# Kernel tuning notes

Hardware: AMD Instinct MI355X
Metric: run time of the kernel (lower is better)

The kernel has to match this reference:

```python
import jax, jax.numpy as jnp
import numpy as np

B, S, D = 4, 512, 256
VOCAB, MAX_RULES = 50257, 1024
EPS = 1e-12  # F.normalize default eps


def setup_inputs() -> dict:
    key = jax.random.key(0)
    k1, k2, k3, k4 = jax.random.split(key, 4)
    hidden_states = jax.random.normal(k1, (B, S, D), dtype=jnp.float32)
    token_ids = jax.random.randint(k2, (B, S), 0, VOCAB, dtype=jnp.int64)
    rule_transform = jax.random.normal(k3, (MAX_RULES, D, D), dtype=jnp.float32)
    token_rules = jax.random.randint(k4, (VOCAB,), 0, MAX_RULES, dtype=jnp.int64)
    return {
        "hidden_states": hidden_states,
        "token_ids": token_ids,
        "rule_transform": rule_transform,
        "token_rules": token_rules,
    }


def reference(hidden_states, token_ids, rule_transform, token_rules):
    # per-token rule index: [B, S]
    rule_indices = token_rules[token_ids]
    # gather DxD rule matrix per token: [B, S, D, D]
    rule_matrices = rule_transform[rule_indices]
    # F.normalize(p=2, dim=(-2,-1)): divide by Frobenius norm per matrix
    fro = jnp.sqrt(jnp.sum(rule_matrices * rule_matrices, axis=(-2, -1), keepdims=True))
    rule_matrices = rule_matrices / jnp.maximum(fro, EPS)
    # batched matvec: [B,S,D] x [B,S,D,E] -> [B,S,E]
    return jnp.einsum("bsd,bsde->bse", hidden_states, rule_matrices)
```

## Files before the change

### kernel.cpp

```cpp
#include <hip/hip_runtime.h>
#include <math.h>

#define D 256
#define NRULES 1024
#define TPB 8
#define KMAX 16

__global__ void prep_kernel(const int* __restrict__ token_ids,
                            const int* __restrict__ token_rules,
                            int ntok,
                            int* __restrict__ counts,
                            int* __restrict__ bucket,
                            int* __restrict__ spill,
                            int* __restrict__ nspill) {
    const int i = blockIdx.x * blockDim.x + threadIdx.x;
    if (i >= ntok) return;
    const int r = token_rules[token_ids[i]];
    const int slot = atomicAdd(&counts[r], 1);
    if (slot < KMAX) bucket[r * KMAX + slot] = i;
    else             spill[atomicAdd(nspill, 1)] = (r << 16) | i;
}

__device__ __forceinline__ void apply_rule(
    const float* __restrict__ M,
    const int* toks,
    int count,
    const float* __restrict__ hidden,
    float* __restrict__ out,
    float (*h_lds)[D], float* sq_lds,
    int t, int wave, int lane, int rr, int col)
{
    for (int base = 0; base < count; base += TPB) {
        #pragma unroll
        for (int j = 0; j < TPB; ++j) {
            const int idx = base + j;
            h_lds[j][t] = (idx < count)
                ? hidden[(size_t)toks[idx] * D + t] : 0.f;
        }
        __syncthreads();

        float4 acc[TPB];
        #pragma unroll
        for (int j = 0; j < TPB; ++j) acc[j] = float4{0.f, 0.f, 0.f, 0.f};
        float sq = 0.f;

        #pragma unroll 8
        for (int i = 0; i < 64; ++i) {
            const int d = (i << 2) + rr;
            const float4 m = *reinterpret_cast<const float4*>(M + (size_t)d * D + col);
            sq = fmaf(m.x, m.x, fmaf(m.y, m.y, fmaf(m.z, m.z, fmaf(m.w, m.w, sq))));
            #pragma unroll
            for (int j = 0; j < TPB; ++j) {
                const float h = h_lds[j][d];
                acc[j].x = fmaf(h, m.x, acc[j].x);
                acc[j].y = fmaf(h, m.y, acc[j].y);
                acc[j].z = fmaf(h, m.z, acc[j].z);
                acc[j].w = fmaf(h, m.w, acc[j].w);
            }
        }

        #pragma unroll
        for (int off = 32; off > 0; off >>= 1)
            sq += __shfl_down(sq, off, 64);
        if (lane == 0) sq_lds[wave] = sq;

        #pragma unroll
        for (int j = 0; j < TPB; ++j) {
            #pragma unroll
            for (int mask = 16; mask < 64; mask <<= 1) {
                acc[j].x += __shfl_xor(acc[j].x, mask, 64);
                acc[j].y += __shfl_xor(acc[j].y, mask, 64);
                acc[j].z += __shfl_xor(acc[j].z, mask, 64);
                acc[j].w += __shfl_xor(acc[j].w, mask, 64);
            }
        }
        __syncthreads();

        const float fro2 = sq_lds[0] + sq_lds[1] + sq_lds[2] + sq_lds[3];
        const float inv  = 1.0f / fmaxf(sqrtf(fro2), 1e-12f);

        #pragma unroll
        for (int j = 0; j < TPB; ++j) {
            if (rr == (j & 3) && base + j < count) {
                const int tok = toks[base + j];
                float4 o;
                o.x = acc[j].x * inv; o.y = acc[j].y * inv;
                o.z = acc[j].z * inv; o.w = acc[j].w * inv;
                *reinterpret_cast<float4*>(out + (size_t)tok * D + col) = o;
            }
        }
        __syncthreads();
    }
}

__global__ __launch_bounds__(256) void process_kernel(
    const float* __restrict__ hidden,
    const float* __restrict__ rules,
    const int*   __restrict__ counts,
    const int*   __restrict__ bucket,
    const int*   __restrict__ spill,
    const int*   __restrict__ nspill,
    float* __restrict__ out)
{
    const int b    = blockIdx.x;
    const int t    = threadIdx.x;
    const int wave = t >> 6;
    const int lane = t & 63;
    const int rr   = lane >> 4;
    const int col  = (wave << 6) + ((lane & 15) << 2);

    __shared__ float h_lds[TPB][D];
    __shared__ float sq_lds[4];
    __shared__ int   toks[KMAX];

    const int cnt = min(counts[b], KMAX);
    if (cnt > 0) {
        if (t < cnt) toks[t] = bucket[b * KMAX + t];
        __syncthreads();
        apply_rule(rules + (size_t)b * D * D, toks, cnt,
                   hidden, out, h_lds, sq_lds, t, wave, lane, rr, col);
    }

    const int ns = nspill[0];
    for (int k = b; k < ns; k += gridDim.x) {
        __syncthreads();
        const int e = spill[k];
        if (t == 0) toks[0] = e & 0xFFFF;
        __syncthreads();
        apply_rule(rules + (size_t)(e >> 16) * D * D, toks, 1,
                   hidden, out, h_lds, sq_lds, t, wave, lane, rr, col);
    }
}

extern "C" void kernel_launch(void* const* d_in, const int* in_sizes, int n_in,
                              void* d_out, int out_size, void* d_ws, size_t ws_size,
                              hipStream_t stream) {
    const float* hidden      = (const float*)d_in[0];
    const int*   token_ids   = (const int*)d_in[1];
    const float* rules       = (const float*)d_in[2];
    const int*   token_rules = (const int*)d_in[3];
    float*       out         = (float*)d_out;

    const int ntok = in_sizes[1];

    int* ws     = (int*)d_ws;
    int* counts = ws;
    int* nspill = ws + NRULES;
    int* bucket = ws + NRULES + 8;
    int* spill  = bucket + NRULES * KMAX;

    hipMemsetAsync(counts, 0, (NRULES + 8) * sizeof(int), stream);
    prep_kernel<<<(ntok + 255) / 256, 256, 0, stream>>>(
        token_ids, token_rules, ntok, counts, bucket, spill, nspill);
    process_kernel<<<NRULES, 256, 0, stream>>>(
        hidden, rules, counts, bucket, spill, nspill, out);
}
```

Before: 50.74 us.

## Split per-rule work into column-quarter units with compacted worklist and separate norm pass

The prep kernel now builds a compacted worklist of (rule, column-quarter) units, so only rules that have tokens launch blocks, and each 64-thread block handles a quarter of the output columns. The Frobenius norm is accumulated per quarter into a buffer and applied by a new elementwise normalization kernel. Compute loops are templated on the actual token count to avoid wasted FMAs on padded slots. The aim is to drop idle blocks, raise parallelism and cut useless work. The cost is an extra kernel launch and an extra read/write pass over the output. The grid size is fixed at 4*NRULES+256, which can cap the number of spill units.

```diff
diff --git a/kernel.cpp b/kernel.cpp
--- a/kernel.cpp
+++ b/kernel.cpp
@@ -11,31 +11,100 @@
                             int ntok,
                             int* __restrict__ counts,
                             int* __restrict__ bucket,
-                            int* __restrict__ spill,
-                            int* __restrict__ nspill) {
+                            int* __restrict__ rule_of_token,
+                            int* __restrict__ worklist,
+                            int* __restrict__ nunits) {
     const int i = blockIdx.x * blockDim.x + threadIdx.x;
     if (i >= ntok) return;
     const int r = token_rules[token_ids[i]];
+    rule_of_token[i] = r;
     const int slot = atomicAdd(&counts[r], 1);
-    if (slot < KMAX) bucket[r * KMAX + slot] = i;
-    else             spill[atomicAdd(nspill, 1)] = (r << 16) | i;
-}
-
-__device__ __forceinline__ void apply_rule(
-    const float* __restrict__ M,
-    const int* toks,
-    int count,
+    if (slot < KMAX) {
+        bucket[r * KMAX + slot] = i;
+        if (slot == 0) {
+            const int w = atomicAdd(nunits, 4);
+            #pragma unroll
+            for (int q = 0; q < 4; ++q) worklist[w + q] = (r << 2) | q;
+        }
+    } else {
+        const int w = atomicAdd(nunits, 4);
+        #pragma unroll
+        for (int q = 0; q < 4; ++q)
+            worklist[w + q] = (int)(0x80000000u | ((unsigned)i << 2) | (unsigned)q);
+    }
+}
+
+template <int CNT>
+__device__ __forceinline__ void quarter_compute(
+    const float* __restrict__ M, const float (*__restrict__ h_lds)[D],
+    int rr, int col, float4* acc, float& sq)
+{
+    #pragma unroll 8
+    for (int i = 0; i < 64; ++i) {
+        const int d = (i << 2) + rr;
+        const float4 m = *reinterpret_cast<const float4*>(M + (size_t)d * D + col);
+        sq = fmaf(m.x, m.x, fmaf(m.y, m.y, fmaf(m.z, m.z, fmaf(m.w, m.w, sq))));
+        #pragma unroll
+        for (int j = 0; j < CNT; ++j) {
+            const float h = h_lds[j][d];
+            acc[j].x = fmaf(h, m.x, acc[j].x);
+            acc[j].y = fmaf(h, m.y, acc[j].y);
+            acc[j].z = fmaf(h, m.z, acc[j].z);
+            acc[j].w = fmaf(h, m.w, acc[j].w);
+        }
+    }
+}
+
+__global__ __launch_bounds__(64) void matvec_kernel(
     const float* __restrict__ hidden,
-    float* __restrict__ out,
-    float (*h_lds)[D], float* sq_lds,
-    int t, int wave, int lane, int rr, int col)
+    const float* __restrict__ rules,
+    const int*   __restrict__ counts,
+    const int*   __restrict__ bucket,
+    const int*   __restrict__ rule_of_token,
+    const int*   __restrict__ worklist,
+    const int*   __restrict__ nunits,
+    float* __restrict__ fro2buf,
+    float* __restrict__ out)
 {
-    for (int base = 0; base < count; base += TPB) {
-        #pragma unroll
-        for (int j = 0; j < TPB; ++j) {
-            const int idx = base + j;
-            h_lds[j][t] = (idx < count)
-                ? hidden[(size_t)toks[idx] * D + t] : 0.f;
+    if ((int)blockIdx.x >= nunits[0]) return;
+    const int e  = worklist[blockIdx.x];
+    const int t  = threadIdx.x;
+    const int rr = t >> 4;
+    const int c4 = (t & 15) << 2;
+
+    __shared__ float h_lds[TPB][D];
+    __shared__ int   toks[KMAX];
+
+    int r, q, cnt;
+    bool owner;
+    if (e < 0) {
+        const int tok = (e & 0x7fffffff) >> 2;
+        q = e & 3;
+        r = rule_of_token[tok];
+        cnt = 1;
+        owner = false;
+        if (t == 0) toks[0] = tok;
+    } else {
+        r = e >> 2; q = e & 3;
+        cnt = min(counts[r], KMAX);
+        owner = true;
+        if (t < cnt) toks[t] = bucket[r * KMAX + t];
+    }
+    __syncthreads();
+
+    const int col = (q << 6) + c4;
+    const float* __restrict__ M = rules + (size_t)r * D * D;
+
+    for (int base = 0; base < cnt; base += TPB) {
+        const int c  = min(cnt - base, TPB);
+        const int cr = (c == 1) ? 1 : (c == 2) ? 2 : (c <= 4) ? 4 : 8;
+
+        for (int j = 0; j < cr; ++j) {
+            float4 v = {0.f, 0.f, 0.f, 0.f};
+            if (j < c)
+                v = *reinterpret_cast<const float4*>(
+                    &hidden[(size_t)toks[base + j] * D + (t << 2)]);
+            *reinterpret_cast<float4*>(&h_lds[j][t << 2]) = v;
         }
         __syncthreads();
 
@@ -44,28 +113,14 @@
         for (int j = 0; j < TPB; ++j) acc[j] = float4{0.f, 0.f, 0.f, 0.f};
         float sq = 0.f;
 
-        #pragma unroll 8
-        for (int i = 0; i < 64; ++i) {
-            const int d = (i << 2) + rr;
-            const float4 m = *reinterpret_cast<const float4*>(M + (size_t)d * D + col);
-            sq = fmaf(m.x, m.x, fmaf(m.y, m.y, fmaf(m.z, m.z, fmaf(m.w, m.w, sq))));
-            #pragma unroll
-            for (int j = 0; j < TPB; ++j) {
-                const float h = h_lds[j][d];
-                acc[j].x = fmaf(h, m.x, acc[j].x);
-                acc[j].y = fmaf(h, m.y, acc[j].y);
-                acc[j].z = fmaf(h, m.z, acc[j].z);
-                acc[j].w = fmaf(h, m.w, acc[j].w);
-            }
-        }
-
-        #pragma unroll
-        for (int off = 32; off > 0; off >>= 1)
-            sq += __shfl_down(sq, off, 64);
-        if (lane == 0) sq_lds[wave] = sq;
-
-        #pragma unroll
-        for (int j = 0; j < TPB; ++j) {
+        switch (cr) {
+            case 1: quarter_compute<1>(M, h_lds, rr, col, acc, sq); break;
+            case 2: quarter_compute<2>(M, h_lds, rr, col, acc, sq); break;
+            case 4: quarter_compute<4>(M, h_lds, rr, col, acc, sq); break;
+            default: quarter_compute<8>(M, h_lds, rr, col, acc, sq); break;
+        }
+
+        for (int j = 0; j < cr; ++j) {
             #pragma unroll
             for (int mask = 16; mask < 64; mask <<= 1) {
                 acc[j].x += __shfl_xor(acc[j].x, mask, 64);
@@ -74,62 +129,42 @@
                 acc[j].w += __shfl_xor(acc[j].w, mask, 64);
             }
         }
+
+        if (owner && base == 0) {
+            float s = sq;
+            #pragma unroll
+            for (int off = 32; off > 0; off >>= 1)
+                s += __shfl_down(s, off, 64);
+            if (t == 0) fro2buf[(r << 2) | q] = s;
+        }
+
+        for (int j = 0; j < cr; ++j) {
+            if (j < c && rr == (j & 3)) {
+                const int tok = toks[base + j];
+                *reinterpret_cast<float4*>(&out[(size_t)tok * D + col]) = acc[j];
+            }
+        }
         __syncthreads();
-
-        const float fro2 = sq_lds[0] + sq_lds[1] + sq_lds[2] + sq_lds[3];
-        const float inv  = 1.0f / fmaxf(sqrtf(fro2), 1e-12f);
-
-        #pragma unroll
-        for (int j = 0; j < TPB; ++j) {
-            if (rr == (j & 3) && base + j < count) {
-                const int tok = toks[base + j];
-                float4 o;
-                o.x = acc[j].x * inv; o.y = acc[j].y * inv;
-                o.z = acc[j].z * inv; o.w = acc[j].w * inv;
-                *reinterpret_cast<float4*>(out + (size_t)tok * D + col) = o;
-            }
-        }
-        __syncthreads();
-    }
-}
-
-__global__ __launch_bounds__(256) void process_kernel(
-    const float* __restrict__ hidden,
-    const float* __restrict__ rules,
-    const int*   __restrict__ counts,
-    const int*   __restrict__ bucket,
-    const int*   __restrict__ spill,
-    const int*   __restrict__ nspill,
-    float* __restrict__ out)
+    }
+}
+
+__global__ __launch_bounds__(256) void norm_kernel(
+    float* __restrict__ out,
+    const int* __restrict__ rule_of_token,
+    const float* __restrict__ fro2buf,
+    int ntok)
 {
-    const int b    = blockIdx.x;
-    const int t    = threadIdx.x;
-    const int wave = t >> 6;
-    const int lane = t & 63;
-    const int rr   = lane >> 4;
-    const int col  = (wave << 6) + ((lane & 15) << 2);
-
-    __shared__ float h_lds[TPB][D];
-    __shared__ float sq_lds[4];
-    __shared__ int   toks[KMAX];
-
-    const int cnt = min(counts[b], KMAX);
-    if (cnt > 0) {
-        if (t < cnt) toks[t] = bucket[b * KMAX + t];
-        __syncthreads();
-        apply_rule(rules + (size_t)b * D * D, toks, cnt,
-                   hidden, out, h_lds, sq_lds, t, wave, lane, rr, col);
-    }
-
-    const int ns = nspill[0];
-    for (int k = b; k < ns; k += gridDim.x) {
-        __syncthreads();
-        const int e = spill[k];
-        if (t == 0) toks[0] = e & 0xFFFF;
-        __syncthreads();
-        apply_rule(rules + (size_t)(e >> 16) * D * D, toks, 1,
-                   hidden, out, h_lds, sq_lds, t, wave, lane, rr, col);
-    }
+    const int g   = blockIdx.x * 256 + threadIdx.x;
+    const int tok = g >> 6;
+    if (tok >= ntok) return;
+    const int c4  = (g & 63) << 2;
+    const int r   = rule_of_token[tok];
+    const float f = fro2buf[r * 4] + fro2buf[r * 4 + 1] +
+                    fro2buf[r * 4 + 2] + fro2buf[r * 4 + 3];
+    const float inv = 1.0f / fmaxf(sqrtf(f), 1e-12f);
+    float4 v = *reinterpret_cast<float4*>(&out[(size_t)tok * D + c4]);
+    v.x *= inv; v.y *= inv; v.z *= inv; v.w *= inv;
+    *reinterpret_cast<float4*>(&out[(size_t)tok * D + c4]) = v;
 }
 
 extern "C" void kernel_launch(void* const* d_in, const int* in_sizes, int n_in,
@@ -143,15 +178,23 @@
 
     const int ntok = in_sizes[1];
 
-    int* ws     = (int*)d_ws;
-    int* counts = ws;
-    int* nspill = ws + NRULES;
-    int* bucket = ws + NRULES + 8;
-    int* spill  = bucket + NRULES * KMAX;
+    int* ws            = (int*)d_ws;
+    int* counts        = ws;
+    int* nunits        = ws + NRULES;
+    int* bucket        = ws + NRULES + 8;
+    int* rule_of_token = bucket + NRULES * KMAX;
+    int* worklist      = rule_of_token + ntok;
+    float* fro2buf     = (float*)(worklist + 4 * NRULES + 1024);
+
+    const int max_units = 4 * NRULES + 256;
 
     hipMemsetAsync(counts, 0, (NRULES + 8) * sizeof(int), stream);
     prep_kernel<<<(ntok + 255) / 256, 256, 0, stream>>>(
-        token_ids, token_rules, ntok, counts, bucket, spill, nspill);
-    process_kernel<<<NRULES, 256, 0, stream>>>(
-        hidden, rules, counts, bucket, spill, nspill, out);
-}
+        token_ids, token_rules, ntok, counts, bucket, rule_of_token,
+        worklist, nunits);
+    matvec_kernel<<<max_units, 64, 0, stream>>>(
+        hidden, rules, counts, bucket, rule_of_token, worklist, nunits,
+        fro2buf, out);
+    norm_kernel<<<(ntok * 64 + 255) / 256, 256, 0, stream>>>(
+        out, rule_of_token, fro2buf, ntok);
+}
```

New measurement: 82.37 us. 1.62x slower.

## Use single-wave blocks with count-specialized rule passes and extra spill blocks

Applied to the files above, without the earlier changes.

Shrinks each per-rule block from four waves to one 64-thread wave that walks all 256 rows, so the cross-wave shuffle reductions and LDS exchange of the squared norm go away. Templates the inner pass on the token count (1/2/4/8) so rules with few tokens avoid wasted FMAs on zero-padded rows. Adds extra blocks dedicated to spilled tokens. In exchange each block streams the whole 256 KB matrix with one wave, which lowers per-block memory-level parallelism and may leave the GPU underfilled.

```diff
diff --git a/kernel.cpp b/kernel.cpp
--- a/kernel.cpp
+++ b/kernel.cpp
@@ -5,6 +5,7 @@
 #define NRULES 1024
 #define TPB 8
 #define KMAX 16
+#define NSPILLBLK 64
 
 __global__ void prep_kernel(const int* __restrict__ token_ids,
                             const int* __restrict__ token_rules,
@@ -21,79 +22,56 @@
     else             spill[atomicAdd(nspill, 1)] = (r << 16) | i;
 }
 
-__device__ __forceinline__ void apply_rule(
+template <int CNT>
+__device__ __forceinline__ void rule_pass(
     const float* __restrict__ M,
-    const int* toks,
-    int count,
-    const float* __restrict__ hidden,
-    float* __restrict__ out,
-    float (*h_lds)[D], float* sq_lds,
-    int t, int wave, int lane, int rr, int col)
+    const float (*__restrict__ h_lds)[D],
+    const int* __restrict__ toks,
+    int c,
+    int t,
+    float* __restrict__ out)
 {
-    for (int base = 0; base < count; base += TPB) {
+    const int c4 = t << 2;
+    float4 acc[CNT];
+    #pragma unroll
+    for (int j = 0; j < CNT; ++j) acc[j] = float4{0.f, 0.f, 0.f, 0.f};
+    float sqx = 0.f, sqy = 0.f, sqz = 0.f, sqw = 0.f;
+
+    #pragma unroll 8
+    for (int d = 0; d < D; ++d) {
+        const float4 m = *reinterpret_cast<const float4*>(M + (size_t)d * D + c4);
+        sqx = fmaf(m.x, m.x, sqx);
+        sqy = fmaf(m.y, m.y, sqy);
+        sqz = fmaf(m.z, m.z, sqz);
+        sqw = fmaf(m.w, m.w, sqw);
         #pragma unroll
-        for (int j = 0; j < TPB; ++j) {
-            const int idx = base + j;
-            h_lds[j][t] = (idx < count)
-                ? hidden[(size_t)toks[idx] * D + t] : 0.f;
+        for (int j = 0; j < CNT; ++j) {
+            const float h = h_lds[j][d];
+            acc[j].x = fmaf(h, m.x, acc[j].x);
+            acc[j].y = fmaf(h, m.y, acc[j].y);
+            acc[j].z = fmaf(h, m.z, acc[j].z);
+            acc[j].w = fmaf(h, m.w, acc[j].w);
         }
-        __syncthreads();
+    }
 
-        float4 acc[TPB];
-        #pragma unroll
-        for (int j = 0; j < TPB; ++j) acc[j] = float4{0.f, 0.f, 0.f, 0.f};
-        float sq = 0.f;
+    float sq = (sqx + sqy) + (sqz + sqw);
+    #pragma unroll
+    for (int mask = 1; mask < 64; mask <<= 1)
+        sq += __shfl_xor(sq, mask, 64);
+    const float inv = 1.0f / fmaxf(sqrtf(sq), 1e-12f);
 
-        #pragma unroll 8
-        for (int i = 0; i < 64; ++i) {
-            const int d = (i << 2) + rr;
-            const float4 m = *reinterpret_cast<const float4*>(M + (size_t)d * D + col);
-            sq = fmaf(m.x, m.x, fmaf(m.y, m.y, fmaf(m.z, m.z, fmaf(m.w, m.w, sq))));
-            #pragma unroll
-            for (int j = 0; j < TPB; ++j) {
-                const float h = h_lds[j][d];
-                acc[j].x = fmaf(h, m.x, acc[j].x);
-                acc[j].y = fmaf(h, m.y, acc[j].y);
-                acc[j].z = fmaf(h, m.z, acc[j].z);
-                acc[j].w = fmaf(h, m.w, acc[j].w);
-            }
+    #pragma unroll
+    for (int j = 0; j < CNT; ++j) {
+        if (j < c) {
+            float4 o;
+            o.x = acc[j].x * inv; o.y = acc[j].y * inv;
+            o.z = acc[j].z * inv; o.w = acc[j].w * inv;
+            *reinterpret_cast<float4*>(&out[(size_t)toks[j] * D + c4]) = o;
         }
-
-        #pragma unroll
-        for (int off = 32; off > 0; off >>= 1)
-            sq += __shfl_down(sq, off, 64);
-        if (lane == 0) sq_lds[wave] = sq;
-
-        #pragma unroll
-        for (int j = 0; j < TPB; ++j) {
-            #pragma unroll
-            for (int mask = 16; mask < 64; mask <<= 1) {
-                acc[j].x += __shfl_xor(acc[j].x, mask, 64);
-                acc[j].y += __shfl_xor(acc[j].y, mask, 64);
-                acc[j].z += __shfl_xor(acc[j].z, mask, 64);
-                acc[j].w += __shfl_xor(acc[j].w, mask, 64);
-            }
-        }
-        __syncthreads();
-
-        const float fro2 = sq_lds[0] + sq_lds[1] + sq_lds[2] + sq_lds[3];
-        const float inv  = 1.0f / fmaxf(sqrtf(fro2), 1e-12f);
-
-        #pragma unroll
-        for (int j = 0; j < TPB; ++j) {
-            if (rr == (j & 3) && base + j < count) {
-                const int tok = toks[base + j];
-                float4 o;
-                o.x = acc[j].x * inv; o.y = acc[j].y * inv;
-                o.z = acc[j].z * inv; o.w = acc[j].w * inv;
-                *reinterpret_cast<float4*>(out + (size_t)tok * D + col) = o;
-            }
-        }
-        __syncthreads();
     }
 }
 
-__global__ __launch_bounds__(256) void process_kernel(
+__global__ __launch_bounds__(64) void process_kernel(
     const float* __restrict__ hidden,
     const float* __restrict__ rules,
     const int*   __restrict__ counts,
@@ -102,33 +80,51 @@
     const int*   __restrict__ nspill,
     float* __restrict__ out)
 {
-    const int b    = blockIdx.x;
-    const int t    = threadIdx.x;
-    const int wave = t >> 6;
-    const int lane = t & 63;
-    const int rr   = lane >> 4;
-    const int col  = (wave << 6) + ((lane & 15) << 2);
+    const int b = blockIdx.x;
+    const int t = threadIdx.x;
 
     __shared__ float h_lds[TPB][D];
-    __shared__ float sq_lds[4];
-    __shared__ int   toks[KMAX];
+    __shared__ int   toks[TPB];
 
-    const int cnt = min(counts[b], KMAX);
-    if (cnt > 0) {
-        if (t < cnt) toks[t] = bucket[b * KMAX + t];
-        __syncthreads();
-        apply_rule(rules + (size_t)b * D * D, toks, cnt,
-                   hidden, out, h_lds, sq_lds, t, wave, lane, rr, col);
+    if (b < NRULES) {
+        const int cnt = min(counts[b], KMAX);
+        if (cnt > 0) {
+            const float* __restrict__ M = rules + (size_t)b * D * D;
+            for (int base = 0; base < cnt; base += TPB) {
+                const int c = min(cnt - base, TPB);
+                if (t < c) toks[t] = bucket[b * KMAX + base + t];
+                #pragma unroll
+                for (int j = 0; j < TPB; ++j) {
+                    float4 v = {0.f, 0.f, 0.f, 0.f};
+                    if (j < c)
+                        v = *reinterpret_cast<const float4*>(
+                            &hidden[(size_t)bucket[b * KMAX + base + j] * D + (t << 2)]);
+                    *reinterpret_cast<float4*>(&h_lds[j][t << 2]) = v;
+                }
+                __syncthreads();
+
+                switch ((c == 1) ? 1 : (c == 2) ? 2 : (c <= 4) ? 4 : 8) {
+                    case 1:  rule_pass<1>(M, h_lds, toks, c, t, out); break;
+                    case 2:  rule_pass<2>(M, h_lds, toks, c, t, out); break;
+                    case 4:  rule_pass<4>(M, h_lds, toks, c, t, out); break;
+                    default: rule_pass<8>(M, h_lds, toks, c, t, out); break;
+                }
+                __syncthreads();
+            }
+        }
     }
 
     const int ns = nspill[0];
     for (int k = b; k < ns; k += gridDim.x) {
         __syncthreads();
-        const int e = spill[k];
-        if (t == 0) toks[0] = e & 0xFFFF;
+        const int e   = spill[k];
+        const int tok = e & 0xFFFF;
+        const int r   = e >> 16;
+        if (t == 0) toks[0] = tok;
+        *reinterpret_cast<float4*>(&h_lds[0][t << 2]) =
+            *reinterpret_cast<const float4*>(&hidden[(size_t)tok * D + (t << 2)]);
         __syncthreads();
-        apply_rule(rules + (size_t)(e >> 16) * D * D, toks, 1,
-                   hidden, out, h_lds, sq_lds, t, wave, lane, rr, col);
+        rule_pass<1>(rules + (size_t)r * D * D, h_lds, toks, 1, t, out);
     }
 }
 
@@ -152,6 +148,6 @@
     hipMemsetAsync(counts, 0, (NRULES + 8) * sizeof(int), stream);
     prep_kernel<<<(ntok + 255) / 256, 256, 0, stream>>>(
         token_ids, token_rules, ntok, counts, bucket, spill, nspill);
-    process_kernel<<<NRULES, 256, 0, stream>>>(
+    process_kernel<<<NRULES + NSPILLBLK, 64, 0, stream>>>(
         hidden, rules, counts, bucket, spill, nspill, out);
 }
```

After: 111.0 us. +118.8%, slower.

## Add atomic worklist of active rules and count-specialized tile passes

Applied to the files above, without the earlier changes.

The prep kernel now records each rule that has tokens into a compact worklist. The process kernel has blocks pull rules from it through an atomic counter instead of launching one block per rule, so empty rules cost nothing. Per-pass token tiles are templated on actual count (1/2/4/8), which cuts wasted FMAs and registers when a rule has few tokens, and hidden loads become float4 wide. The cost is a global atomic per work item, a larger code footprint from template instantiations, and a work-stealing loop that only pays off when many rules are empty or lightly loaded.

```diff
diff --git a/kernel.cpp b/kernel.cpp
--- a/kernel.cpp
+++ b/kernel.cpp
@@ -11,86 +11,91 @@
                             int ntok,
                             int* __restrict__ counts,
                             int* __restrict__ bucket,
-                            int* __restrict__ spill,
-                            int* __restrict__ nspill) {
+                            int* __restrict__ worklist,
+                            int* __restrict__ ctrl,
+                            int* __restrict__ spill) {
     const int i = blockIdx.x * blockDim.x + threadIdx.x;
     if (i >= ntok) return;
     const int r = token_rules[token_ids[i]];
     const int slot = atomicAdd(&counts[r], 1);
-    if (slot < KMAX) bucket[r * KMAX + slot] = i;
-    else             spill[atomicAdd(nspill, 1)] = (r << 16) | i;
+    if (slot < KMAX) {
+        bucket[r * KMAX + slot] = i;
+        if (slot == 0) worklist[atomicAdd(&ctrl[0], 1)] = r;
+    } else {
+        spill[atomicAdd(&ctrl[2], 1)] = (r << 16) | i;
+    }
 }
 
-__device__ __forceinline__ void apply_rule(
+template <int CR>
+__device__ __forceinline__ void do_pass(
     const float* __restrict__ M,
-    const int* toks,
-    int count,
     const float* __restrict__ hidden,
-    float* __restrict__ out,
-    float (*h_lds)[D], float* sq_lds,
-    int t, int wave, int lane, int rr, int col)
+    const int* bucketrow,
+    int base, int c,
+    int t, int wave, int lane, int rr, int col,
+    float (*__restrict__ h_lds)[D], float* __restrict__ sq_lds,
+    float* __restrict__ out)
 {
-    for (int base = 0; base < count; base += TPB) {
+    for (int j = wave; j < CR; j += 4) {
+        float4 v = {0.f, 0.f, 0.f, 0.f};
+        if (j < c)
+            v = *reinterpret_cast<const float4*>(
+                &hidden[(size_t)bucketrow[base + j] * D + (lane << 2)]);
+        *reinterpret_cast<float4*>(&h_lds[j][lane << 2]) = v;
+    }
+    __syncthreads();
+
+    float4 acc[CR];
+    #pragma unroll
+    for (int j = 0; j < CR; ++j) acc[j] = float4{0.f, 0.f, 0.f, 0.f};
+    float sq = 0.f;
+
+    #pragma unroll 8
+    for (int i = 0; i < 64; ++i) {
+        const int d = (i << 2) + rr;
+        const float4 m = *reinterpret_cast<const float4*>(M + (size_t)d * D + col);
+        sq = fmaf(m.x, m.x, fmaf(m.y, m.y, fmaf(m.z, m.z, fmaf(m.w, m.w, sq))));
         #pragma unroll
-        for (int j = 0; j < TPB; ++j) {
-            const int idx = base + j;
-            h_lds[j][t] = (idx < count)
-                ? hidden[(size_t)toks[idx] * D + t] : 0.f;
+        for (int j = 0; j < CR; ++j) {
+            const float h = h_lds[j][d];
+            acc[j].x = fmaf(h, m.x, acc[j].x);
+            acc[j].y = fmaf(h, m.y, acc[j].y);
+            acc[j].z = fmaf(h, m.z, acc[j].z);
+            acc[j].w = fmaf(h, m.w, acc[j].w);
         }
-        __syncthreads();
+    }
 
-        float4 acc[TPB];
+    #pragma unroll
+    for (int off = 32; off > 0; off >>= 1)
+        sq += __shfl_down(sq, off, 64);
+    if (lane == 0) sq_lds[wave] = sq;
+
+    #pragma unroll
+    for (int j = 0; j < CR; ++j) {
         #pragma unroll
-        for (int j = 0; j < TPB; ++j) acc[j] = float4{0.f, 0.f, 0.f, 0.f};
-        float sq = 0.f;
+        for (int mask = 16; mask < 64; mask <<= 1) {
+            acc[j].x += __shfl_xor(acc[j].x, mask, 64);
+            acc[j].y += __shfl_xor(acc[j].y, mask, 64);
+            acc[j].z += __shfl_xor(acc[j].z, mask, 64);
+            acc[j].w += __shfl_xor(acc[j].w, mask, 64);
+        }
+    }
+    __syncthreads();
 
-        #pragma unroll 8
-        for (int i = 0; i < 64; ++i) {
-            const int d = (i << 2) + rr;
-            const float4 m = *reinterpret_cast<const float4*>(M + (size_t)d * D + col);
-            sq = fmaf(m.x, m.x, fmaf(m.y, m.y, fmaf(m.z, m.z, fmaf(m.w, m.w, sq))));
-            #pragma unroll
-            for (int j = 0; j < TPB; ++j) {
-                const float h = h_lds[j][d];
-                acc[j].x = fmaf(h, m.x, acc[j].x);
-                acc[j].y = fmaf(h, m.y, acc[j].y);
-                acc[j].z = fmaf(h, m.z, acc[j].z);
-                acc[j].w = fmaf(h, m.w, acc[j].w);
-            }
+    const float fro2 = sq_lds[0] + sq_lds[1] + sq_lds[2] + sq_lds[3];
+    const float inv  = 1.0f / fmaxf(sqrtf(fro2), 1e-12f);
+
+    #pragma unroll
+    for (int j = 0; j < CR; ++j) {
+        if (j < c && rr == (j & 3)) {
+            const int tok = bucketrow[base + j];
+            float4 o;
+            o.x = acc[j].x * inv; o.y = acc[j].y * inv;
+            o.z = acc[j].z * inv; o.w = acc[j].w * inv;
+            *reinterpret_cast<float4*>(&out[(size_t)tok * D + col]) = o;
         }
-
-        #pragma unroll
-        for (int off = 32; off > 0; off >>= 1)
-            sq += __shfl_down(sq, off, 64);
-        if (lane == 0) sq_lds[wave] = sq;
-
-        #pragma unroll
-        for (int j = 0; j < TPB; ++j) {
-            #pragma unroll
-            for (int mask = 16; mask < 64; mask <<= 1) {
-                acc[j].x += __shfl_xor(acc[j].x, mask, 64);
-                acc[j].y += __shfl_xor(acc[j].y, mask, 64);
-                acc[j].z += __shfl_xor(acc[j].z, mask, 64);
-                acc[j].w += __shfl_xor(acc[j].w, mask, 64);
-            }
-        }
-        __syncthreads();
-
-        const float fro2 = sq_lds[0] + sq_lds[1] + sq_lds[2] + sq_lds[3];
-        const float inv  = 1.0f / fmaxf(sqrtf(fro2), 1e-12f);
-
-        #pragma unroll
-        for (int j = 0; j < TPB; ++j) {
-            if (rr == (j & 3) && base + j < count) {
-                const int tok = toks[base + j];
-                float4 o;
-                o.x = acc[j].x * inv; o.y = acc[j].y * inv;
-                o.z = acc[j].z * inv; o.w = acc[j].w * inv;
-                *reinterpret_cast<float4*>(out + (size_t)tok * D + col) = o;
-            }
-        }
-        __syncthreads();
     }
+    __syncthreads();
 }
 
 __global__ __launch_bounds__(256) void process_kernel(
@@ -98,11 +103,11 @@
     const float* __restrict__ rules,
     const int*   __restrict__ counts,
     const int*   __restrict__ bucket,
+    const int*   __restrict__ worklist,
+    int*         __restrict__ ctrl,
     const int*   __restrict__ spill,
-    const int*   __restrict__ nspill,
     float* __restrict__ out)
 {
-    const int b    = blockIdx.x;
     const int t    = threadIdx.x;
     const int wave = t >> 6;
     const int lane = t & 63;
@@ -111,24 +116,40 @@
 
     __shared__ float h_lds[TPB][D];
     __shared__ float sq_lds[4];
-    __shared__ int   toks[KMAX];
+    __shared__ int   sh_w;
+    __shared__ int   stok[1];
 
-    const int cnt = min(counts[b], KMAX);
-    if (cnt > 0) {
-        if (t < cnt) toks[t] = bucket[b * KMAX + t];
+    const int nwork = ctrl[0];
+
+    for (;;) {
+        if (t == 0) sh_w = atomicAdd(&ctrl[1], 1);
         __syncthreads();
-        apply_rule(rules + (size_t)b * D * D, toks, cnt,
-                   hidden, out, h_lds, sq_lds, t, wave, lane, rr, col);
+        const int w = sh_w;
+        if (w >= nwork) break;
+
+        const int r   = worklist[w];
+        const int cnt = min(counts[r], KMAX);
+        const float* __restrict__ M = rules + (size_t)r * D * D;
+        const int* brow = &bucket[r * KMAX];
+
+        for (int base = 0; base < cnt; base += TPB) {
+            const int c = min(cnt - base, TPB);
+            switch ((c == 1) ? 1 : (c == 2) ? 2 : (c <= 4) ? 4 : 8) {
+                case 1:  do_pass<1>(M, hidden, brow, base, c, t, wave, lane, rr, col, h_lds, sq_lds, out); break;
+                case 2:  do_pass<2>(M, hidden, brow, base, c, t, wave, lane, rr, col, h_lds, sq_lds, out); break;
+                case 4:  do_pass<4>(M, hidden, brow, base, c, t, wave, lane, rr, col, h_lds, sq_lds, out); break;
+                default: do_pass<8>(M, hidden, brow, base, c, t, wave, lane, rr, col, h_lds, sq_lds, out); break;
+            }
+        }
     }
 
-    const int ns = nspill[0];
-    for (int k = b; k < ns; k += gridDim.x) {
+    const int ns = ctrl[2];
+    for (int k = blockIdx.x; k < ns; k += gridDim.x) {
+        const int e = spill[k];
+        if (t == 0) stok[0] = e & 0xFFFF;
         __syncthreads();
-        const int e = spill[k];
-        if (t == 0) toks[0] = e & 0xFFFF;
-        __syncthreads();
-        apply_rule(rules + (size_t)(e >> 16) * D * D, toks, 1,
-                   hidden, out, h_lds, sq_lds, t, wave, lane, rr, col);
+        do_pass<1>(rules + (size_t)(e >> 16) * D * D, hidden, stok, 0, 1,
+                   t, wave, lane, rr, col, h_lds, sq_lds, out);
     }
 }
 
@@ -143,15 +164,16 @@
 
     const int ntok = in_sizes[1];
 
-    int* ws     = (int*)d_ws;
-    int* counts = ws;
-    int* nspill = ws + NRULES;
-    int* bucket = ws + NRULES + 8;
-    int* spill  = bucket + NRULES * KMAX;
+    int* ws       = (int*)d_ws;
+    int* counts   = ws;
+    int* ctrl     = ws + NRULES;
+    int* bucket   = ws + NRULES + 8;
+    int* worklist = bucket + NRULES * KMAX;
+    int* spill    = worklist + NRULES;
 
     hipMemsetAsync(counts, 0, (NRULES + 8) * sizeof(int), stream);
     prep_kernel<<<(ntok + 255) / 256, 256, 0, stream>>>(
-        token_ids, token_rules, ntok, counts, bucket, spill, nspill);
+        token_ids, token_rules, ntok, counts, bucket, worklist, ctrl, spill);
     process_kernel<<<NRULES, 256, 0, stream>>>(
-        hidden, rules, counts, bucket, spill, nspill, out);
+        hidden, rules, counts, bucket, worklist, ctrl, spill, out);
 }
```

After: 86.00 us. +69.5%, slower.
